# Performance work log

Hardware: AMD Instinct MI355X
Metric: run time of the kernel (lower is better)

Reference implementation:

```python
import jax, jax.numpy as jnp
import numpy as np

H = 16            # num_heads
SEG = 2048        # segment_size
DIL = 8           # dilation_rate
BLOCK_M = 64      # triton query block size (min(64, M_padded))


def setup_inputs() -> dict:
    key = jax.random.key(0)
    k1, k2, k3 = jax.random.split(key, 3)
    B, M, D = 2, 8192, 1024
    x = jax.random.normal(k1, (B, M, D), dtype=jnp.float32)
    Wqkv = jax.random.normal(k2, (3 * D, D), dtype=jnp.float32) * 0.02
    Wout = jax.random.normal(k3, (D, D), dtype=jnp.float32) * 0.02
    return {"x": x, "Wqkv": Wqkv, "Wout": Wout}


def reference(x, Wqkv, Wout):
    B, M, D = x.shape
    hd = D // H
    scale = hd ** -0.5
    S = M // SEG                      # number of segments (M is a multiple of SEG)
    Kn = SEG // DIL                   # dilated keys per segment
    nb = SEG // BLOCK_M               # query blocks per segment

    # qkv projection (torch Linear: x @ W^T), split into q,k,v: [B,H,M,hd]
    qkv = jnp.einsum('bmd,ed->bme', x, Wqkv).reshape(B, M, 3, H, hd)
    qkv = jnp.transpose(qkv, (2, 0, 3, 1, 4))
    q, k, v = qkv[0] * scale, qkv[1], qkv[2]

    # segment-local views
    q4 = q.reshape(B, H, S, SEG, hd)
    k4 = k.reshape(B, H, S, SEG, hd)[:, :, :, ::DIL]   # [B,H,S,Kn,hd] dilated keys
    v4 = v.reshape(B, H, S, SEG, hd)[:, :, :, ::DIL]

    # scores per segment: [B,H,S,SEG,Kn]
    scores = jnp.einsum('bhspd,bhskd->bhspk', q4, k4)
    # kernel normalization: per key j, subtract max over the 64-query block
    scores = scores.reshape(B, H, S, nb, BLOCK_M, Kn)
    c = jnp.max(scores, axis=4, keepdims=True)          # [B,H,S,nb,1,Kn]
    w = jnp.exp(scores - c)
    den = jnp.sum(w, axis=-1) + 1e-10                   # [B,H,S,nb,BLOCK_M]
    num = jnp.einsum('bhsnmk,bhskd->bhsnmd', w, v4)
    out = num / den[..., None]                          # [B,H,S,nb,BLOCK_M,hd]

    out = out.reshape(B, H, M, hd)
    out = jnp.transpose(out, (0, 2, 1, 3)).reshape(B, M, D)
    return jnp.einsum('bmd,ed->bme', out, Wout)
```

## Files before the change

kernel.cpp:

```cpp
#include <hip/hip_runtime.h>
#include <hip/hip_bf16.h>
#include <stdint.h>


typedef __attribute__((ext_vector_type(8))) short short8;
typedef __attribute__((ext_vector_type(4))) float f32x4;
typedef __attribute__((ext_vector_type(4))) unsigned short ushort4v;

#define DEVI static __device__ __forceinline__

DEVI unsigned short f2bf(float f) {
  union { float f; uint32_t u; } v; v.f = f;
  return (unsigned short)((v.u + 0x7FFFu + ((v.u >> 16) & 1u)) >> 16);
}

DEVI uint32_t pack_bf16(float lo, float hi) {
  return (uint32_t)f2bf(lo) | ((uint32_t)f2bf(hi) << 16);
}

DEVI void gload_lds16(const void* g, void* l) {
  __builtin_amdgcn_global_load_lds((const __attribute__((address_space(1))) void*)g,
                                   (__attribute__((address_space(3))) void*)l,
                                   16, 0, 0);
}

__global__ void cvt_kernel(const float* __restrict__ in, unsigned short* __restrict__ out, int n) {
  int i = (blockIdx.x * 256 + threadIdx.x) * 4;
  if (i >= n) return;
  float4 f = *(const float4*)(in + i);
  uint2 o;
  o.x = (uint32_t)f2bf(f.x) | ((uint32_t)f2bf(f.y) << 16);
  o.y = (uint32_t)f2bf(f.z) | ((uint32_t)f2bf(f.w) << 16);
  *(uint2*)(out + i) = o;
}

#define STAGE_A(bf, hf, kt) do { \
  gload_lds16(Abase + (long)((hf) * 128 + srow0) * 1024 + (kt) * 64 + scol0, &smA[bf][hf][se0]); \
  gload_lds16(Abase + (long)((hf) * 128 + srow1) * 1024 + (kt) * 64 + scol1, &smA[bf][hf][se1]); \
} while (0)
#define STAGE_B(bf, hf, kt) do { \
  gload_lds16(Bbase + (long)((hf) * 128 + srow0) * 1024 + (kt) * 64 + scol0, &smB[bf][hf][se0]); \
  gload_lds16(Bbase + (long)((hf) * 128 + srow1) * 1024 + (kt) * 64 + scol1, &smB[bf][hf][se1]); \
} while (0)

template<bool OUT_F32>
__global__ __launch_bounds__(512, 1) void gemm8p(
    const unsigned short* __restrict__ A, const unsigned short* __restrict__ B,
    void* __restrict__ Cv, float scale)
{
  __shared__ unsigned short smA[2][2][128 * 64];
  __shared__ unsigned short smB[2][2][128 * 64];
  const int tid = threadIdx.x;
  const int tm = blockIdx.x, tn = blockIdx.y;
  const int w = tid >> 6, lane = tid & 63;
  const int wm = w >> 2, wn = w & 3;
  const int lr = lane & 15, lq = lane >> 4;

  const int e0 = tid * 8,        e1 = (512 + tid) * 8;
  const int srow0 = e0 >> 6,     srow1 = e1 >> 6;
  const int sc0 = (e0 >> 3) & 7, sc1 = (e1 >> 3) & 7;
  const int scol0 = (sc0 ^ (srow0 & 7)) * 8, scol1 = (sc1 ^ (srow1 & 7)) * 8;
  const int se0 = e0, se1 = e1;

  const unsigned short* Abase = A + (long)tm * 256 * 1024;
  const unsigned short* Bbase = B + (long)tn * 256 * 1024;

  f32x4 acc[8][4] = {};
  short8 af[4][2];
  short8 bfr[2][2];

  STAGE_A(0, 0, 0); STAGE_B(0, 0, 0); STAGE_B(0, 1, 0); STAGE_A(0, 1, 0);
  asm volatile("s_waitcnt vmcnt(4)" ::: "memory");
  __builtin_amdgcn_s_barrier();
  asm volatile("" ::: "memory");

  for (int t = 0; t < 8; ++t) {
#pragma unroll
    for (int p = 0; p < 8; ++p) {
      const int o = p >> 2;
      const int q = p & 3;
      const int a = (p >> 1) & 1;
      const int b = a ^ (q & 1);

      if ((q & 1) == 0) {
#pragma unroll
        for (int mi2 = 0; mi2 < 4; ++mi2) {
          int r = wm * 64 + mi2 * 16 + lr;
#pragma unroll
          for (int kk = 0; kk < 2; ++kk) {
            int kc = kk * 4 + lq;
            af[mi2][kk] = *(const short8*)&smA[o][a][r * 64 + ((kc ^ (r & 7)) * 8)];
          }
        }
      }
      if (q != 2) {
#pragma unroll
        for (int nj2 = 0; nj2 < 2; ++nj2) {
          int r = wn * 32 + nj2 * 16 + lr;
#pragma unroll
          for (int kk = 0; kk < 2; ++kk) {
            int kc = kk * 4 + lq;
            bfr[nj2][kk] = *(const short8*)&smB[o][b][r * 64 + ((kc ^ (r & 7)) * 8)];
          }
        }
      }

      switch (p) {
        case 0: STAGE_A(1, 0, 2 * t + 1); STAGE_B(1, 0, 2 * t + 1); break;
        case 1: STAGE_B(1, 1, 2 * t + 1); break;
        case 2: STAGE_A(1, 1, 2 * t + 1); break;
        case 4: if (t < 7) { STAGE_A(0, 0, 2 * t + 2); STAGE_B(0, 0, 2 * t + 2); } break;
        case 5: if (t < 7) STAGE_B(0, 1, 2 * t + 2); break;
        case 6: if (t < 7) STAGE_A(0, 1, 2 * t + 2); break;
      }

      asm volatile("s_waitcnt lgkmcnt(0)" ::: "memory");
      __builtin_amdgcn_sched_barrier(0);

      __builtin_amdgcn_s_setprio(1);
#pragma unroll
      for (int kk = 0; kk < 2; ++kk)
#pragma unroll
        for (int mi2 = 0; mi2 < 4; ++mi2)
#pragma unroll
          for (int nj2 = 0; nj2 < 2; ++nj2)
            acc[a * 4 + mi2][b * 2 + nj2] = __builtin_amdgcn_mfma_f32_16x16x32_bf16(
                af[mi2][kk], bfr[nj2][kk], acc[a * 4 + mi2][b * 2 + nj2], 0, 0, 0);
      __builtin_amdgcn_s_setprio(0);

      if (t < 7 || p < 4) {
        asm volatile("s_waitcnt vmcnt(4)" ::: "memory");
      } else if (p == 4) {
        asm volatile("s_waitcnt vmcnt(2)" ::: "memory");
      } else {
        asm volatile("s_waitcnt vmcnt(0)" ::: "memory");
      }
      __builtin_amdgcn_s_barrier();
      asm volatile("" ::: "memory");
    }
  }

  const int row0 = tm * 256 + wm * 64 + lq * 4;
  const int col0 = tn * 256 + wn * 32 + lr;
#pragma unroll
  for (int mi = 0; mi < 8; ++mi) {
    int row = row0 + (mi & 3) * 16 + (mi >> 2) * 128;
#pragma unroll
    for (int nj = 0; nj < 4; ++nj) {
      int col = col0 + (nj & 1) * 16 + (nj >> 1) * 128;
#pragma unroll
      for (int rr = 0; rr < 4; ++rr) {
        float v = acc[mi][nj][rr] * scale;
        long off = (long)(row + rr) * 1024 + col;
        if (OUT_F32) ((float*)Cv)[off] = v;
        else         ((unsigned short*)Cv)[off] = f2bf(v);
      }
    }
  }
}

template<int EPI>
__global__ __launch_bounds__(256, 2) void gemm_bt(
    const unsigned short* __restrict__ A, const unsigned short* __restrict__ B,
    void* __restrict__ Cv, unsigned short* __restrict__ Cv2,
    float scale, long a_row_stride, int ldc, int K)
{
  __shared__ unsigned short smA[128 * 64];
  __shared__ unsigned short smB[128 * 64];
  const int tid = threadIdx.x;
  const int tm = blockIdx.x, tn = blockIdx.y;
  const int w = tid >> 6, lane = tid & 63;
  const int wr = (w >> 1) * 64, wc = (w & 1) * 64;
  const int lr = lane & 15, lq = lane >> 4;

  int se[4], srow[4], scol[4];
#pragma unroll
  for (int i = 0; i < 4; ++i) {
    int e = (i * 256 + tid) * 8;
    int r = e >> 6;
    int cc = (e >> 3) & 7;
    se[i] = e; srow[i] = r; scol[i] = (cc ^ (r & 7)) * 8;
  }

  f32x4 acc[4][4] = {};

  for (int kt = 0; kt < K / 64; ++kt) {
    if (kt) __syncthreads();
#pragma unroll
    for (int i = 0; i < 4; ++i)
      gload_lds16(A + (long)(tm * 128 + srow[i]) * a_row_stride + kt * 64 + scol[i], &smA[se[i]]);
#pragma unroll
    for (int i = 0; i < 4; ++i)
      gload_lds16(B + (long)(tn * 128 + srow[i]) * K + kt * 64 + scol[i], &smB[se[i]]);
    __syncthreads();

#pragma unroll
    for (int kk = 0; kk < 2; ++kk) {
      int kc = kk * 4 + lq;
      short8 af[4], bfm[4];
#pragma unroll
      for (int i = 0; i < 4; ++i) {
        int row = wr + i * 16 + lr;
        af[i] = *(const short8*)&smA[row * 64 + ((kc ^ (row & 7)) * 8)];
      }
#pragma unroll
      for (int j = 0; j < 4; ++j) {
        int row = wc + j * 16 + lr;
        bfm[j] = *(const short8*)&smB[row * 64 + ((kc ^ (row & 7)) * 8)];
      }
#pragma unroll
      for (int i = 0; i < 4; ++i)
#pragma unroll
        for (int j = 0; j < 4; ++j)
          acc[i][j] = __builtin_amdgcn_mfma_f32_16x16x32_bf16(af[i], bfm[j], acc[i][j], 0, 0, 0);
    }
  }

  if (EPI == 2 && tn >= 8) {
    const int fbase = (tn - 8) * 128 + wc;
#pragma unroll
    for (int ip = 0; ip < 4; ip += 2) {
      int t0 = tm * 128 + wr + ip * 16 + lq * 4;
      int seg = t0 >> 8;
      int ts  = t0 & 255;
      int c32 = (ts >> 5) * 16 + (ts & 15);
#pragma unroll
      for (int j = 0; j < 4; ++j) {
        int f = fbase + j * 16 + lr;
        uint32_t* rp = (uint32_t*)&Cv2[((long)(seg * 1024 + f)) * 256];
        uint4 U;
        U.x = pack_bf16(acc[ip][j][0] * scale, acc[ip + 1][j][0] * scale);
        U.y = pack_bf16(acc[ip][j][1] * scale, acc[ip + 1][j][1] * scale);
        U.z = pack_bf16(acc[ip][j][2] * scale, acc[ip + 1][j][2] * scale);
        U.w = pack_bf16(acc[ip][j][3] * scale, acc[ip + 1][j][3] * scale);
        *(uint4*)&rp[c32] = U;
      }
    }
    return;
  }

#pragma unroll
  for (int i = 0; i < 4; ++i) {
    int rg0 = tm * 128 + wr + i * 16 + lq * 4;
#pragma unroll
    for (int j = 0; j < 4; ++j) {
      int cg = tn * 128 + wc + j * 16 + lr;
#pragma unroll
      for (int r = 0; r < 4; ++r) {
        float v = acc[i][j][r] * scale;
        long off = (long)(rg0 + r) * ldc + cg;
        if (EPI == 0) ((float*)Cv)[off] = v;
        else          ((unsigned short*)Cv)[off] = f2bf(v);
      }
    }
  }
}

__global__ __launch_bounds__(256, 2) void attn_kernel(
    const unsigned short* __restrict__ qb,
    const unsigned short* __restrict__ kb,
    const unsigned short* __restrict__ vtb,
    unsigned short* __restrict__ attout)
{
  __shared__ unsigned short v_t[64 * 256];
  __shared__ uint32_t w32[4][64][18];

  const int u = (blockIdx.x & 7) * 128 + (blockIdx.x >> 3);
  const int e8 = u & 7, h = (u >> 3) & 15, s = (u >> 7) & 3, b = u >> 9;
  const int tid = threadIdx.x, w = tid >> 6, lane = tid & 63;
  const int lr = lane & 15, lq = lane >> 4;
  const long qrow0 = (long)b * 8192 + s * 2048 + e8 * 256 + w * 64;
  const int hc = h * 64;

  const unsigned short* kbase = kb + ((long)(b * 4 + s) * 256) * 1024 + hc;
  const unsigned short* vbase = vtb + ((long)(b * 4 + s) * 1024 + hc) * 256;

#pragma unroll
  for (int it = 0; it < 8; ++it) {
    int e = (it * 256 + tid) * 8;
    int f = e >> 8;
    int ch = (e >> 3) & 31;
    gload_lds16(vbase + (long)f * 256 + ((ch ^ (f & 7)) * 8), &v_t[e]);
  }

  const unsigned short* qbase = qb + qrow0 * 1024 + hc;
  short8 aq[4][2];
#pragma unroll
  for (int i = 0; i < 4; ++i)
#pragma unroll
    for (int kk = 0; kk < 2; ++kk)
      aq[i][kk] = *(const short8*)&qbase[(i * 16 + lr) * 1024 + (kk * 4 + lq) * 8];

  __syncthreads();

  short8 ones;
#pragma unroll
  for (int e = 0; e < 8; ++e) ones[e] = (short)0x3F80;

  uint32_t (*wsl)[18] = w32[w];

  f32x4 acc_pv[4][4] = {};
  f32x4 acc_den[4] = {};

  short8 bkc[2][2], bkn[2][2];
#pragma unroll
  for (int j = 0; j < 2; ++j)
#pragma unroll
    for (int kk = 0; kk < 2; ++kk)
      bkc[j][kk] = *(const short8*)&kbase[(long)(j * 16 + lr) * 1024 + (kk * 4 + lq) * 8];

#pragma unroll
  for (int c = 0; c < 8; ++c) {
    if (c < 7) {
#pragma unroll
      for (int j = 0; j < 2; ++j)
#pragma unroll
        for (int kk = 0; kk < 2; ++kk)
          bkn[j][kk] = *(const short8*)
            &kbase[(long)((c + 1) * 32 + j * 16 + lr) * 1024 + (kk * 4 + lq) * 8];
    }

    f32x4 acc_s[4][2] = {};
#pragma unroll
    for (int kk = 0; kk < 2; ++kk)
#pragma unroll
      for (int i = 0; i < 4; ++i)
#pragma unroll
        for (int j = 0; j < 2; ++j)
          acc_s[i][j] = __builtin_amdgcn_mfma_f32_16x16x32_bf16(aq[i][kk], bkc[j][kk], acc_s[i][j], 0, 0, 0);

    float cmax[2];
#pragma unroll
    for (int j = 0; j < 2; ++j) {
      float m = -3.4e38f;
#pragma unroll
      for (int i = 0; i < 4; ++i)
#pragma unroll
        for (int r = 0; r < 4; ++r) m = fmaxf(m, acc_s[i][j][r]);
      m = fmaxf(m, __shfl_xor(m, 16));
      m = fmaxf(m, __shfl_xor(m, 32));
      cmax[j] = m;
    }

#pragma unroll
    for (int i = 0; i < 4; ++i) {
#pragma unroll
      for (int r = 0; r < 4; ++r) {
        int q = i * 16 + lq * 4 + r;
        wsl[q][lr] = pack_bf16(exp2f(acc_s[i][0][r] - cmax[0]),
                               exp2f(acc_s[i][1][r] - cmax[1]));
      }
    }

    short8 av[4];
#pragma unroll
    for (int ct = 0; ct < 4; ++ct) {
      int frow = ct * 16 + lr;
      av[ct] = *(const short8*)&v_t[frow * 256 + (((c * 4 + lq) ^ (frow & 7)) << 3)];
    }
#pragma unroll
    for (int qi = 0; qi < 4; ++qi) {
      short8 bw = *(const short8*)&wsl[qi * 16 + lr][lq * 4];
      acc_den[qi] = __builtin_amdgcn_mfma_f32_16x16x32_bf16(ones, bw, acc_den[qi], 0, 0, 0);
#pragma unroll
      for (int ct = 0; ct < 4; ++ct)
        acc_pv[qi][ct] = __builtin_amdgcn_mfma_f32_16x16x32_bf16(av[ct], bw, acc_pv[qi][ct], 0, 0, 0);
    }

#pragma unroll
    for (int j = 0; j < 2; ++j)
#pragma unroll
      for (int kk = 0; kk < 2; ++kk)
        bkc[j][kk] = bkn[j][kk];
  }

#pragma unroll
  for (int qi = 0; qi < 4; ++qi) {
    float inv = 1.0f / (acc_den[qi][0] + 1e-10f);
    long orow = (qrow0 + qi * 16 + lr) * 1024 + hc;
#pragma unroll
    for (int ct = 0; ct < 4; ++ct) {
      ushort4v p;
#pragma unroll
      for (int r = 0; r < 4; ++r) p[r] = f2bf(acc_pv[qi][ct][r] * inv);
      *(ushort4v*)&attout[orow + ct * 16 + lq * 4] = p;
    }
  }
}

extern "C" void kernel_launch(void* const* d_in, const int* in_sizes, int n_in,
                              void* d_out, int out_size, void* d_ws, size_t ws_size,
                              hipStream_t stream) {
  (void)in_sizes; (void)n_in; (void)out_size; (void)ws_size;
  const float* x    = (const float*)d_in[0];
  const float* Wqkv = (const float*)d_in[1];
  const float* Wout = (const float*)d_in[2];
  float* out = (float*)d_out;
  char* ws = (char*)d_ws;

  unsigned short* xb     = (unsigned short*)(ws);
  unsigned short* attout = (unsigned short*)(ws);
  unsigned short* wqkvb  = (unsigned short*)(ws + 33554432);
  unsigned short* woutb  = (unsigned short*)(ws + 39845888);
  unsigned short* qbuf   = (unsigned short*)(ws + 41943040);
  unsigned short* kbuf   = (unsigned short*)(ws + 75497472);
  unsigned short* vtb    = (unsigned short*)(ws + 79691776);

  cvt_kernel<<<16384, 256, 0, stream>>>(x, xb, 16777216);
  cvt_kernel<<<3072, 256, 0, stream>>>(Wqkv, wqkvb, 3 * 1024 * 1024);
  cvt_kernel<<<1024, 256, 0, stream>>>(Wout, woutb, 1024 * 1024);

  gemm8p<false><<<dim3(64, 4), 512, 0, stream>>>(xb, wqkvb, (void*)qbuf,
                                                 0.125f * 1.44269504088896340736f);
  gemm_bt<2><<<dim3(16, 16), 256, 0, stream>>>(
      xb, wqkvb + 1024 * 1024, (void*)kbuf, vtb, 1.0f, 8192, 1024, 1024);

  attn_kernel<<<1024, 256, 0, stream>>>(qbuf, kbuf, vtb, attout);

  gemm8p<true><<<dim3(64, 4), 512, 0, stream>>>(attout, woutb, (void*)out, 1.0f);
}
```

Measured before the change: 171.5 us.

## Software-pipeline attention QK^T with softmax-PV, enlarge blocks, refine GEMM B-fragment reuse

The attention kernel now runs 512-thread blocks over 512 query rows, which halves the number of blocks that reload the shared V tile. Its key-chunk loop is unrolled into a ping-pong pipeline, so the QK^T MFMAs for the next chunk are issued alongside the softmax and PV work of the current one. Exp2 with a log2e-scaled Q is replaced by __expf with an unscaled Q, and the w32 padding grows to 20. In the projection GEMM, B fragments are double-buffered by half so fewer LDS reads and lgkm waits are needed, and the vmcnt waits are loosened. This adds register pressure, and the relaxed wait counts risk correctness if they are miscounted.

```diff
diff --git a/kernel.cpp b/kernel.cpp
--- a/kernel.cpp
+++ b/kernel.cpp
@@ -67,7 +67,7 @@
 
   f32x4 acc[8][4] = {};
   short8 af[4][2];
-  short8 bfr[2][2];
+  short8 bfr[2][2][2];
 
   STAGE_A(0, 0, 0); STAGE_B(0, 0, 0); STAGE_B(0, 1, 0); STAGE_A(0, 1, 0);
   asm volatile("s_waitcnt vmcnt(4)" ::: "memory");
@@ -82,7 +82,7 @@
       const int a = (p >> 1) & 1;
       const int b = a ^ (q & 1);
 
-      if ((q & 1) == 0) {
+      if (q == 0 || q == 2) {
 #pragma unroll
         for (int mi2 = 0; mi2 < 4; ++mi2) {
           int r = wm * 64 + mi2 * 16 + lr;
@@ -93,14 +93,14 @@
           }
         }
       }
-      if (q != 2) {
+      if (q == 0 || q == 1) {
 #pragma unroll
         for (int nj2 = 0; nj2 < 2; ++nj2) {
           int r = wn * 32 + nj2 * 16 + lr;
 #pragma unroll
           for (int kk = 0; kk < 2; ++kk) {
             int kc = kk * 4 + lq;
-            bfr[nj2][kk] = *(const short8*)&smB[o][b][r * 64 + ((kc ^ (r & 7)) * 8)];
+            bfr[b][nj2][kk] = *(const short8*)&smB[o][b][r * 64 + ((kc ^ (r & 7)) * 8)];
           }
         }
       }
@@ -114,8 +114,10 @@
         case 6: if (t < 7) STAGE_A(0, 1, 2 * t + 2); break;
       }
 
-      asm volatile("s_waitcnt lgkmcnt(0)" ::: "memory");
-      __builtin_amdgcn_sched_barrier(0);
+      if (q != 3) {
+        asm volatile("s_waitcnt lgkmcnt(0)" ::: "memory");
+        __builtin_amdgcn_sched_barrier(0);
+      }
 
       __builtin_amdgcn_s_setprio(1);
 #pragma unroll
@@ -125,15 +127,19 @@
 #pragma unroll
           for (int nj2 = 0; nj2 < 2; ++nj2)
             acc[a * 4 + mi2][b * 2 + nj2] = __builtin_amdgcn_mfma_f32_16x16x32_bf16(
-                af[mi2][kk], bfr[nj2][kk], acc[a * 4 + mi2][b * 2 + nj2], 0, 0, 0);
+                af[mi2][kk], bfr[b][nj2][kk], acc[a * 4 + mi2][b * 2 + nj2], 0, 0, 0);
       __builtin_amdgcn_s_setprio(0);
 
-      if (t < 7 || p < 4) {
-        asm volatile("s_waitcnt vmcnt(4)" ::: "memory");
-      } else if (p == 4) {
-        asm volatile("s_waitcnt vmcnt(2)" ::: "memory");
+      if (t < 7) {
+        if (p == 0 || p == 1 || p == 4 || p == 5)
+          asm volatile("s_waitcnt vmcnt(6)" ::: "memory");
+        else if (p == 3 || p == 7)
+          asm volatile("s_waitcnt vmcnt(4)" ::: "memory");
       } else {
-        asm volatile("s_waitcnt vmcnt(0)" ::: "memory");
+        if (p == 0 || p == 1)      asm volatile("s_waitcnt vmcnt(6)" ::: "memory");
+        else if (p == 3)           asm volatile("s_waitcnt vmcnt(4)" ::: "memory");
+        else if (p == 4)           asm volatile("s_waitcnt vmcnt(2)" ::: "memory");
+        else if (p == 5)           asm volatile("s_waitcnt vmcnt(0)" ::: "memory");
       }
       __builtin_amdgcn_s_barrier();
       asm volatile("" ::: "memory");
@@ -256,28 +262,28 @@
   }
 }
 
-__global__ __launch_bounds__(256, 2) void attn_kernel(
+__global__ __launch_bounds__(512, 2) void attn_kernel(
     const unsigned short* __restrict__ qb,
     const unsigned short* __restrict__ kb,
     const unsigned short* __restrict__ vtb,
     unsigned short* __restrict__ attout)
 {
   __shared__ unsigned short v_t[64 * 256];
-  __shared__ uint32_t w32[4][64][18];
-
-  const int u = (blockIdx.x & 7) * 128 + (blockIdx.x >> 3);
-  const int e8 = u & 7, h = (u >> 3) & 15, s = (u >> 7) & 3, b = u >> 9;
+  __shared__ uint32_t w32[8][64][20];
+
+  const int u = (blockIdx.x & 7) * 64 + (blockIdx.x >> 3);
+  const int quarter = u & 3, h = (u >> 2) & 15, s = (u >> 6) & 3, b = u >> 8;
   const int tid = threadIdx.x, w = tid >> 6, lane = tid & 63;
   const int lr = lane & 15, lq = lane >> 4;
-  const long qrow0 = (long)b * 8192 + s * 2048 + e8 * 256 + w * 64;
+  const long qrow0 = (long)b * 8192 + s * 2048 + quarter * 512 + w * 64;
   const int hc = h * 64;
 
   const unsigned short* kbase = kb + ((long)(b * 4 + s) * 256) * 1024 + hc;
   const unsigned short* vbase = vtb + ((long)(b * 4 + s) * 1024 + hc) * 256;
 
 #pragma unroll
-  for (int it = 0; it < 8; ++it) {
-    int e = (it * 256 + tid) * 8;
+  for (int it = 0; it < 4; ++it) {
+    int e = (it * 512 + tid) * 8;
     int f = e >> 8;
     int ch = (e >> 3) & 31;
     gload_lds16(vbase + (long)f * 256 + ((ch ^ (f & 7)) * 8), &v_t[e]);
@@ -297,82 +303,63 @@
 #pragma unroll
   for (int e = 0; e < 8; ++e) ones[e] = (short)0x3F80;
 
-  uint32_t (*wsl)[18] = w32[w];
+  uint32_t (*wsl)[20] = w32[w];
 
   f32x4 acc_pv[4][4] = {};
   f32x4 acc_den[4] = {};
-
-  short8 bkc[2][2], bkn[2][2];
-#pragma unroll
-  for (int j = 0; j < 2; ++j)
-#pragma unroll
-    for (int kk = 0; kk < 2; ++kk)
-      bkc[j][kk] = *(const short8*)&kbase[(long)(j * 16 + lr) * 1024 + (kk * 4 + lq) * 8];
-
-#pragma unroll
-  for (int c = 0; c < 8; ++c) {
-    if (c < 7) {
-#pragma unroll
-      for (int j = 0; j < 2; ++j)
-#pragma unroll
-        for (int kk = 0; kk < 2; ++kk)
-          bkn[j][kk] = *(const short8*)
-            &kbase[(long)((c + 1) * 32 + j * 16 + lr) * 1024 + (kk * 4 + lq) * 8];
-    }
-
-    f32x4 acc_s[4][2] = {};
-#pragma unroll
-    for (int kk = 0; kk < 2; ++kk)
-#pragma unroll
-      for (int i = 0; i < 4; ++i)
-#pragma unroll
-        for (int j = 0; j < 2; ++j)
-          acc_s[i][j] = __builtin_amdgcn_mfma_f32_16x16x32_bf16(aq[i][kk], bkc[j][kk], acc_s[i][j], 0, 0, 0);
-
-    float cmax[2];
-#pragma unroll
-    for (int j = 0; j < 2; ++j) {
-      float m = -3.4e38f;
-#pragma unroll
-      for (int i = 0; i < 4; ++i)
-#pragma unroll
-        for (int r = 0; r < 4; ++r) m = fmaxf(m, acc_s[i][j][r]);
-      m = fmaxf(m, __shfl_xor(m, 16));
-      m = fmaxf(m, __shfl_xor(m, 32));
-      cmax[j] = m;
-    }
-
-#pragma unroll
-    for (int i = 0; i < 4; ++i) {
-#pragma unroll
-      for (int r = 0; r < 4; ++r) {
-        int q = i * 16 + lq * 4 + r;
-        wsl[q][lr] = pack_bf16(exp2f(acc_s[i][0][r] - cmax[0]),
-                               exp2f(acc_s[i][1][r] - cmax[1]));
-      }
-    }
-
-    short8 av[4];
-#pragma unroll
-    for (int ct = 0; ct < 4; ++ct) {
-      int frow = ct * 16 + lr;
-      av[ct] = *(const short8*)&v_t[frow * 256 + (((c * 4 + lq) ^ (frow & 7)) << 3)];
-    }
-#pragma unroll
-    for (int qi = 0; qi < 4; ++qi) {
-      short8 bw = *(const short8*)&wsl[qi * 16 + lr][lq * 4];
-      acc_den[qi] = __builtin_amdgcn_mfma_f32_16x16x32_bf16(ones, bw, acc_den[qi], 0, 0, 0);
-#pragma unroll
-      for (int ct = 0; ct < 4; ++ct)
-        acc_pv[qi][ct] = __builtin_amdgcn_mfma_f32_16x16x32_bf16(av[ct], bw, acc_pv[qi][ct], 0, 0, 0);
-    }
-
-#pragma unroll
-    for (int j = 0; j < 2; ++j)
-#pragma unroll
-      for (int kk = 0; kk < 2; ++kk)
-        bkc[j][kk] = bkn[j][kk];
-  }
+  short8 bk0[2][2], bk1[2][2];
+  f32x4 sA[4][2], sB[4][2];
+
+#define LOADK(BK, CC) do { \
+  _Pragma("unroll") for (int j = 0; j < 2; ++j) \
+    _Pragma("unroll") for (int kk = 0; kk < 2; ++kk) \
+      BK[j][kk] = *(const short8*)&kbase[(long)((CC) * 32 + j * 16 + lr) * 1024 + (kk * 4 + lq) * 8]; \
+} while (0)
+
+#define QKT(S, BK) do { \
+  _Pragma("unroll") for (int i = 0; i < 4; ++i) \
+    _Pragma("unroll") for (int j = 0; j < 2; ++j) { \
+      f32x4 z = {0.f, 0.f, 0.f, 0.f}; S[i][j] = z; } \
+  _Pragma("unroll") for (int kk = 0; kk < 2; ++kk) \
+    _Pragma("unroll") for (int i = 0; i < 4; ++i) \
+      _Pragma("unroll") for (int j = 0; j < 2; ++j) \
+        S[i][j] = __builtin_amdgcn_mfma_f32_16x16x32_bf16(aq[i][kk], BK[j][kk], S[i][j], 0, 0, 0); \
+} while (0)
+
+#define SOFTPV(S, CC) do { \
+  float c0 = -3.4e38f, c1 = -3.4e38f; \
+  _Pragma("unroll") for (int i = 0; i < 4; ++i) \
+    _Pragma("unroll") for (int r = 0; r < 4; ++r) { \
+      c0 = fmaxf(c0, S[i][0][r]); c1 = fmaxf(c1, S[i][1][r]); } \
+  c0 = fmaxf(c0, __shfl_xor(c0, 16)); c0 = fmaxf(c0, __shfl_xor(c0, 32)); \
+  c1 = fmaxf(c1, __shfl_xor(c1, 16)); c1 = fmaxf(c1, __shfl_xor(c1, 32)); \
+  _Pragma("unroll") for (int i = 0; i < 4; ++i) \
+    _Pragma("unroll") for (int r = 0; r < 4; ++r) { \
+      int qq = i * 16 + lq * 4 + r; \
+      wsl[qq][lr] = pack_bf16(__expf(S[i][0][r] - c0), __expf(S[i][1][r] - c1)); } \
+  short8 av_[4]; \
+  _Pragma("unroll") for (int ct = 0; ct < 4; ++ct) { \
+    int frow = ct * 16 + lr; \
+    av_[ct] = *(const short8*)&v_t[frow * 256 + ((((CC) * 4 + lq) ^ (frow & 7)) << 3)]; } \
+  _Pragma("unroll") for (int qi = 0; qi < 4; ++qi) { \
+    short8 bw = *(const short8*)&wsl[qi * 16 + lr][lq * 4]; \
+    acc_den[qi] = __builtin_amdgcn_mfma_f32_16x16x32_bf16(ones, bw, acc_den[qi], 0, 0, 0); \
+    _Pragma("unroll") for (int ct = 0; ct < 4; ++ct) \
+      acc_pv[qi][ct] = __builtin_amdgcn_mfma_f32_16x16x32_bf16(av_[ct], bw, acc_pv[qi][ct], 0, 0, 0); } \
+} while (0)
+
+  LOADK(bk0, 0);
+  LOADK(bk1, 1);
+  QKT(sA, bk0);
+
+  LOADK(bk0, 2); QKT(sB, bk1); SOFTPV(sA, 0);
+  LOADK(bk1, 3); QKT(sA, bk0); SOFTPV(sB, 1);
+  LOADK(bk0, 4); QKT(sB, bk1); SOFTPV(sA, 2);
+  LOADK(bk1, 5); QKT(sA, bk0); SOFTPV(sB, 3);
+  LOADK(bk0, 6); QKT(sB, bk1); SOFTPV(sA, 4);
+  LOADK(bk1, 7); QKT(sA, bk0); SOFTPV(sB, 5);
+                 QKT(sB, bk1); SOFTPV(sA, 6);
+                               SOFTPV(sB, 7);
 
 #pragma unroll
   for (int qi = 0; qi < 4; ++qi) {
@@ -410,12 +397,11 @@
   cvt_kernel<<<3072, 256, 0, stream>>>(Wqkv, wqkvb, 3 * 1024 * 1024);
   cvt_kernel<<<1024, 256, 0, stream>>>(Wout, woutb, 1024 * 1024);
 
-  gemm8p<false><<<dim3(64, 4), 512, 0, stream>>>(xb, wqkvb, (void*)qbuf,
-                                                 0.125f * 1.44269504088896340736f);
+  gemm8p<false><<<dim3(64, 4), 512, 0, stream>>>(xb, wqkvb, (void*)qbuf, 0.125f);
   gemm_bt<2><<<dim3(16, 16), 256, 0, stream>>>(
       xb, wqkvb + 1024 * 1024, (void*)kbuf, vtb, 1.0f, 8192, 1024, 1024);
 
-  attn_kernel<<<1024, 256, 0, stream>>>(qbuf, kbuf, vtb, attout);
+  attn_kernel<<<512, 512, 0, stream>>>(qbuf, kbuf, vtb, attout);
 
   gemm8p<true><<<dim3(64, 4), 512, 0, stream>>>(attout, woutb, (void*)out, 1.0f);
 }
```

Measured after the change: 165.9 us. 1.03x faster.
